# Performance work log

Measured on AMD Instinct MI355X. Metric: run time of the kernel, lower is better.

## Reference

```python
import jax, jax.numpy as jnp
import numpy as np

NT = 128          # num_timesteps (reference query points)
E = 128           # embed_time
H = 128           # nhidden
NH = 1            # num_heads
F = 32            # feature_size
NS = 2            # num_states
EPS = 1e-5


def layer_norm(x, g, b):
    m = jnp.mean(x, axis=-1, keepdims=True)
    v = jnp.mean((x - m) ** 2, axis=-1, keepdims=True)
    return (x - m) * jax.lax.rsqrt(v + EPS) * g + b


def setup_inputs() -> dict:
    key = jax.random.key(0)
    ks = jax.random.split(key, 24)
    nrm = lambda k, s: (jax.random.normal(k, s) * 0.05).astype(jnp.float32)
    inp = {
        "input": jax.random.normal(ks[0], (8, F, 512), dtype=jnp.float32),
        "mask": jax.random.randint(ks[1], (8, F, 512), 0, 2).astype(jnp.float32),
        "timesteps": jnp.sort(jax.random.uniform(ks[2], (8, 512), dtype=jnp.float32), axis=-1),
        # time embedding
        "periodic_w": nrm(ks[3], (E - 1, 1)), "periodic_b": nrm(ks[4], (E - 1,)),
        "lin_w": nrm(ks[5], (1, 1)), "lin_b": nrm(ks[6], (1,)),
        # query / key projections + layer norms
        "q_w": nrm(ks[7], (E, E)), "q_b": nrm(ks[8], (E,)),
        "q_g": jnp.ones((E,), jnp.float32), "q_be": jnp.zeros((E,), jnp.float32),
        "k_w": nrm(ks[9], (E, E)), "k_b": nrm(ks[10], (E,)),
        "k_g": jnp.ones((E,), jnp.float32), "k_be": jnp.zeros((E,), jnp.float32),
        # attention_norm over h*2F channels, then output linear + LN to nhidden
        "attn_g": jnp.ones((NH * 2 * F,), jnp.float32), "attn_b": jnp.zeros((NH * 2 * F,), jnp.float32),
        "out_w": nrm(ks[11], (H, NH * 2 * F)), "out_b": nrm(ks[12], (H,)),
        "out_g": jnp.ones((H,), jnp.float32), "out_be": jnp.zeros((H,), jnp.float32),
        # GRU (torch gate order r, z, n)
        "gru_wih": nrm(ks[13], (3 * H, H)), "gru_whh": nrm(ks[14], (3 * H, H)),
        "gru_bih": nrm(ks[15], (3 * H,)), "gru_bhh": nrm(ks[16], (3 * H,)),
        # classifier MLP
        "c1_w": nrm(ks[17], (H, H)), "c1_b": nrm(ks[18], (H,)),
        "c2_w": nrm(ks[19], (H, H)), "c2_b": nrm(ks[20], (H,)),
        "c3_w": nrm(ks[21], (NS, H)), "c3_b": nrm(ks[22], (NS,)),
    }
    return inp


def time_embedding(tt, lin_w, lin_b, periodic_w, periodic_b):
    t = tt[..., None]                                   # (..., 1)
    out1 = t @ lin_w.T + lin_b                          # (..., 1)
    out2 = jnp.sin(t @ periodic_w.T + periodic_b)       # (..., E-1)
    return jnp.concatenate([out1, out2], axis=-1)       # (..., E)


def reference(input, mask, timesteps, periodic_w, periodic_b, lin_w, lin_b,
              q_w, q_b, q_g, q_be, k_w, k_b, k_g, k_be,
              attn_g, attn_b, out_w, out_b, out_g, out_be,
              gru_wih, gru_whh, gru_bih, gru_bhh,
              c1_w, c1_b, c2_w, c2_b, c3_w, c3_b):
    B = input.shape[0]
    x_in = jnp.transpose(input, (0, 2, 1))              # (B, T, F)
    m = 1.0 - jnp.transpose(mask, (0, 2, 1))            # (B, T, F)
    x_in = x_in * (m > 0).astype(x_in.dtype)
    x = jnp.concatenate([x_in, m], axis=-1)             # (B, T, 2F)
    mk = jnp.concatenate([m, m], axis=-1)               # (B, T, 2F)

    key_e = time_embedding(timesteps, lin_w, lin_b, periodic_w, periodic_b)        # (B, T, E)
    qtimes = jnp.linspace(0.0, 1.0, NT)
    query_e = time_embedding(qtimes[None], lin_w, lin_b, periodic_w, periodic_b)   # (1, NT, E)

    q = layer_norm(query_e @ q_w.T + q_b, q_g, q_be)    # (1, NT, E)
    k = layer_norm(key_e @ k_w.T + k_b, k_g, k_be)      # (B, T, E)

    etk = E // NH
    q = q.reshape(1, NT, NH, etk).transpose(0, 2, 1, 3)         # (1, h, NT, etk)
    k = k.reshape(B, -1, NH, etk).transpose(0, 2, 1, 3)         # (B, h, T, etk)

    scores = jnp.einsum("ahqd,bhkd->bhqk", q, k) / np.sqrt(etk)  # (B, h, NT, T)
    # per-channel masked softmax over keys: (B, h, NT, T, 2F)
    logits = jnp.where(mk[:, None, None, :, :] == 0, -1e9, scores[..., None])
    p_attn = jax.nn.softmax(logits, axis=-2)
    att = jnp.sum(p_attn * x[:, None, None, :, :], axis=-2)     # (B, h, NT, 2F)

    x2 = att.transpose(0, 2, 1, 3).reshape(B, NT, NH * 2 * F)
    x2 = layer_norm(x2, attn_g, attn_b)
    out = layer_norm(x2 @ out_w.T + out_b, out_g, out_be)       # (B, NT, H)

    # GRU over the NT reference timesteps, last hidden state
    seq = out.transpose(1, 0, 2)                                # (NT, B, H)
    h0 = jnp.zeros((B, H), out.dtype)

    def gru_step(h, x_t):
        gi = x_t @ gru_wih.T + gru_bih
        gh = h @ gru_whh.T + gru_bhh
        ir, iz, inn = jnp.split(gi, 3, axis=-1)
        hr, hz, hn = jnp.split(gh, 3, axis=-1)
        r = jax.nn.sigmoid(ir + hr)
        z = jax.nn.sigmoid(iz + hz)
        n = jnp.tanh(inn + r * hn)
        h_new = (1.0 - z) * n + z * h
        return h_new, None

    h_last, _ = jax.lax.scan(gru_step, h0, seq)

    h1 = jax.nn.relu(h_last @ c1_w.T + c1_b)
    h2 = jax.nn.relu(h1 @ c2_w.T + c2_b)
    return h2 @ c3_w.T + c3_b                                   # (B, num_states) logits
```

## Files before the change

### kernel.cpp

```cpp
#include <hip/hip_runtime.h>
#include <math.h>

#define LN_EPS 1e-5f

typedef _Float16 h2v __attribute__((ext_vector_type(2)));

__device__ __forceinline__ float dot4(float4 a, float4 b) {
    return a.x*b.x + a.y*b.y + a.z*b.z + a.w*b.w;
}
__device__ __forceinline__ void fma4(float4& a, float s, float4 v) {
    a.x += s*v.x; a.y += s*v.y; a.z += s*v.z; a.w += s*v.w;
}
__device__ __forceinline__ float fast_rcp(float x) {
    return __builtin_amdgcn_rcpf(x);
}
__device__ __forceinline__ float fast_sigmoid(float x) {
    return fast_rcp(1.f + __expf(-x));
}
__device__ __forceinline__ float fast_tanh(float x) {
    return 1.f - 2.f*fast_rcp(__expf(2.f*x) + 1.f);
}
__device__ __forceinline__ float fdot2u(unsigned int a, unsigned int b, float c) {
#if __has_builtin(__builtin_amdgcn_fdot2)
    return __builtin_amdgcn_fdot2(__builtin_bit_cast(h2v, a),
                                  __builtin_bit_cast(h2v, b), c, false);
#else
    const h2v av = __builtin_bit_cast(h2v, a);
    const h2v bv = __builtin_bit_cast(h2v, b);
    return c + (float)av[0]*(float)bv[0] + (float)av[1]*(float)bv[1];
#endif
}
__device__ __forceinline__ float wsum64(float v) {
    #pragma unroll
    for (int off = 32; off > 0; off >>= 1) v += __shfl_xor(v, off);
    return v;
}
__device__ __forceinline__ float qadd_xor1(float v) {
    const int x = __builtin_amdgcn_mov_dpp(__builtin_bit_cast(int, v),
                                           0xB1 , 0xF, 0xF, true);
    return v + __builtin_bit_cast(float, x);
}

__global__ void k_embed_proj(
    const float* __restrict__ input, const float* __restrict__ mask,
    const float* __restrict__ timesteps,
    const float* __restrict__ pw, const float* __restrict__ pb,
    const float* __restrict__ lw, const float* __restrict__ lb,
    const float* __restrict__ q_w, const float* __restrict__ q_b,
    const float* __restrict__ q_g, const float* __restrict__ q_be,
    const float* __restrict__ k_w, const float* __restrict__ k_b,
    const float* __restrict__ k_g, const float* __restrict__ k_be,
    float* __restrict__ qs, float* __restrict__ kT, float2* __restrict__ xm)
{
    const int blk = blockIdx.x;
    const int tid = threadIdx.x;

    __shared__ __align__(16) float e[4][128];
    __shared__ __align__(16) float4 red[128];
    __shared__ __align__(16) float proj[4][128];
    __shared__ __align__(16) float2 tile[32][65];

    if (blk < 64) {
        const int b  = blk >> 3;
        const int t0 = (blk & 7) * 64;
        const int cg = tid >> 6;
        const int tt = tid & 63;
        #pragma unroll
        for (int c16 = 0; c16 < 16; ++c16) {
            const int c = c16*2 + cg;
            const float m = mask [(size_t)(b*32 + c)*512 + t0 + tt];
            const float x = input[(size_t)(b*32 + c)*512 + t0 + tt];
            const float mm = 1.0f - m;
            tile[c][tt] = make_float2(x*mm, mm);
        }
        __syncthreads();
        const int c2 = tid & 31;
        const int tg = tid >> 5;
        #pragma unroll
        for (int k = 0; k < 16; ++k) {
            const int t = tg*16 + k;
            xm[((size_t)b*512 + t0 + t)*32 + c2] = tile[c2][t];
        }
        return;
    }

    const bool isq = blk < 96;
    float tv[4];
    int kidx0 = 0;
    if (isq) {
        const int q0 = (blk - 64) * 4;
        #pragma unroll
        for (int r = 0; r < 4; ++r) tv[r] = (float)(q0 + r) * (1.0f/127.0f);
    } else {
        kidx0 = (blk - 96) * 4;
        #pragma unroll
        for (int r = 0; r < 4; ++r) tv[r] = timesteps[kidx0 + r];
    }

    float pwj = 0.f, pbj = 0.f;
    if (tid > 0) { pwj = pw[tid-1]; pbj = pb[tid-1]; }
    const float lw0 = lw[0], lb0 = lb[0];
    #pragma unroll
    for (int r = 0; r < 4; ++r)
        e[r][tid] = (tid == 0) ? (tv[r]*lw0 + lb0) : sinf(tv[r]*pwj + pbj);
    __syncthreads();

    const float* W  = isq ? q_w  : k_w;
    const float* Bv = isq ? q_b  : k_b;
    const float* G  = isq ? q_g  : k_g;
    const float* Be = isq ? q_be : k_be;

    {
        const int jj = tid >> 2, dc = tid & 3;
        const float4* e0 = (const float4*)(&e[0][0]);
        const float4* e1 = (const float4*)(&e[1][0]);
        const float4* e2 = (const float4*)(&e[2][0]);
        const float4* e3 = (const float4*)(&e[3][0]);
        #pragma unroll
        for (int jb = 0; jb < 4; ++jb) {
            const int j = jb*32 + jj;
            const float4* wrow = (const float4*)(W + (size_t)j*128);
            float a0=0.f, a1=0.f, a2=0.f, a3=0.f;
            #pragma unroll
            for (int k = 0; k < 8; ++k) {
                const int idx = dc + 4*k;
                const float4 w4 = wrow[idx];
                a0 += dot4(w4, e0[idx]);
                a1 += dot4(w4, e1[idx]);
                a2 += dot4(w4, e2[idx]);
                a3 += dot4(w4, e3[idx]);
            }
            a0 += __shfl_xor(a0, 1, 4); a0 += __shfl_xor(a0, 2, 4);
            a1 += __shfl_xor(a1, 1, 4); a1 += __shfl_xor(a1, 2, 4);
            a2 += __shfl_xor(a2, 1, 4); a2 += __shfl_xor(a2, 2, 4);
            a3 += __shfl_xor(a3, 1, 4); a3 += __shfl_xor(a3, 2, 4);
            if (dc == 0) {
                const float bj = Bv[j];
                proj[0][j] = a0 + bj; proj[1][j] = a1 + bj;
                proj[2][j] = a2 + bj; proj[3][j] = a3 + bj;
            }
        }
    }
    __syncthreads();

    float acc[4];
    #pragma unroll
    for (int r = 0; r < 4; ++r) acc[r] = proj[r][tid];

    red[tid] = make_float4(acc[0], acc[1], acc[2], acc[3]);
    __syncthreads();
    for (int s = 64; s > 0; s >>= 1) {
        if (tid < s) {
            float4 m = red[tid]; const float4 o = red[tid+s];
            m.x += o.x; m.y += o.y; m.z += o.z; m.w += o.w;
            red[tid] = m;
        }
        __syncthreads();
    }
    float4 mean = red[0];
    mean.x *= (1.0f/128.0f); mean.y *= (1.0f/128.0f);
    mean.z *= (1.0f/128.0f); mean.w *= (1.0f/128.0f);
    __syncthreads();
    const float d0 = acc[0]-mean.x, d1 = acc[1]-mean.y,
                d2 = acc[2]-mean.z, d3 = acc[3]-mean.w;
    red[tid] = make_float4(d0*d0, d1*d1, d2*d2, d3*d3);
    __syncthreads();
    for (int s = 64; s > 0; s >>= 1) {
        if (tid < s) {
            float4 m = red[tid]; const float4 o = red[tid+s];
            m.x += o.x; m.y += o.y; m.z += o.z; m.w += o.w;
            red[tid] = m;
        }
        __syncthreads();
    }
    float4 var = red[0];
    var.x *= (1.0f/128.0f); var.y *= (1.0f/128.0f);
    var.z *= (1.0f/128.0f); var.w *= (1.0f/128.0f);

    const float gg = G[tid], bb = Be[tid];
    const float o0 = d0*rsqrtf(var.x+LN_EPS)*gg + bb;
    const float o1 = d1*rsqrtf(var.y+LN_EPS)*gg + bb;
    const float o2 = d2*rsqrtf(var.z+LN_EPS)*gg + bb;
    const float o3 = d3*rsqrtf(var.w+LN_EPS)*gg + bb;

    if (isq) {
        const float sc = 0.08838834764831845f;
        const int q0 = (blk - 64)*4;
        qs[(size_t)(q0+0)*128 + tid] = o0*sc;
        qs[(size_t)(q0+1)*128 + tid] = o1*sc;
        qs[(size_t)(q0+2)*128 + tid] = o2*sc;
        qs[(size_t)(q0+3)*128 + tid] = o3*sc;
    } else {
        const int b = kidx0 >> 9;
        const int t = kidx0 & 511;
        *(float4*)(kT + ((size_t)(b*128 + tid))*512 + t) =
            make_float4(o0, o1, o2, o3);
    }
}

__global__ void __launch_bounds__(256) k_attn(
    const float2* __restrict__ xm,
    const float* __restrict__ qs, const float* __restrict__ kT,
    const float* __restrict__ attn_g, const float* __restrict__ attn_b,
    const float* __restrict__ out_w, const float* __restrict__ out_b,
    const float* __restrict__ out_g, const float* __restrict__ out_be,
    float* __restrict__ outm)
{
    const int b     = blockIdx.x >> 5;
    const int qbase = (blockIdx.x & 31) * 4;
    const int tid   = threadIdx.x;

    __shared__ __align__(16) float et[4][512];
    __shared__ __align__(16) float qsh[4][128];
    __shared__ __align__(16) float wsh[128*66];
    __shared__ __align__(16) float sA[4][8][32];
    __shared__ __align__(16) float aA[4][8][32];
    __shared__ __align__(16) float x2s[4][64];
    __shared__ float redC[4];

    for (int idx = tid; idx < 512; idx += 256)
        qsh[idx >> 7][idx & 127] = qs[(size_t)(qbase + (idx >> 7))*128 + (idx & 127)];
    for (int idx = tid; idx < 8192; idx += 256)
        wsh[(idx >> 6)*66 + (idx & 63)] = out_w[idx];
    __syncthreads();

    {
        const int grp = tid >> 7;
        const int tl  = tid & 127;
        const int q0  = grp*2;
        const float4* kp  = (const float4*)kT + (size_t)b*128*128 + tl;
        const float4* qa4 = (const float4*)qsh[q0];
        const float4* qb4 = (const float4*)qsh[q0+1];
        float4 a0 = make_float4(0,0,0,0), a1 = make_float4(0,0,0,0);
        float4 c0 = kp[0], c1 = kp[128], c2 = kp[256], c3 = kp[384];
        for (int c = 0; c < 32; ++c) {
            float4 n0, n1, n2, n3;
            if (c < 31) {
                const float4* kn = kp + (size_t)(4*c+4)*128;
                n0 = kn[0]; n1 = kn[128]; n2 = kn[256]; n3 = kn[384];
            }
            const float4 qa = qa4[c], qb = qb4[c];
            fma4(a0, qa.x, c0); fma4(a1, qb.x, c0);
            fma4(a0, qa.y, c1); fma4(a1, qb.y, c1);
            fma4(a0, qa.z, c2); fma4(a1, qb.z, c2);
            fma4(a0, qa.w, c3); fma4(a1, qb.w, c3);
            c0 = n0; c1 = n1; c2 = n2; c3 = n3;
        }
        a0.x = __expf(a0.x); a0.y = __expf(a0.y); a0.z = __expf(a0.z); a0.w = __expf(a0.w);
        a1.x = __expf(a1.x); a1.y = __expf(a1.y); a1.z = __expf(a1.z); a1.w = __expf(a1.w);
        ((float4*)et[q0])[tl]   = a0;
        ((float4*)et[q0+1])[tl] = a1;
    }
    __syncthreads();

    {
        const int c   = tid & 31;
        const int seg = tid >> 5;
        const float2* xp = xm + ((size_t)b*512 + seg*64)*32 + c;
        float s0=0,s1=0,s2=0,s3=0, a0=0,a1=0,a2=0,a3=0;
        #pragma unroll 4
        for (int i = 0; i < 64; ++i) {
            const float2 v = xp[(size_t)i*32];
            const int t = seg*64 + i;
            const float w0 = et[0][t]*v.y, w1 = et[1][t]*v.y;
            const float w2 = et[2][t]*v.y, w3 = et[3][t]*v.y;
            s0 += w0; s1 += w1; s2 += w2; s3 += w3;
            a0 += w0*v.x; a1 += w1*v.x; a2 += w2*v.x; a3 += w3*v.x;
        }
        sA[0][seg][c]=s0; sA[1][seg][c]=s1; sA[2][seg][c]=s2; sA[3][seg][c]=s3;
        aA[0][seg][c]=a0; aA[1][seg][c]=a1; aA[2][seg][c]=a2; aA[3][seg][c]=a3;
    }
    __syncthreads();

    {
        const int ql = tid >> 6;
        const int c2 = tid & 63;
        const int cc = c2 & 31;
        float ss = 0.f;
        #pragma unroll
        for (int g = 0; g < 8; ++g) ss += sA[ql][g][cc];
        float attv;
        if (c2 < 32) {
            float aa = 0.f;
            #pragma unroll
            for (int g = 0; g < 8; ++g) aa += aA[ql][g][cc];
            attv = (ss > 0.f) ? aa/ss : 0.f;
        } else {
            attv = (ss > 0.f) ? 1.0f : 0.0f;
        }
        const float mean = wsum64(attv) * (1.0f/64.0f);
        const float dv = attv - mean;
        const float var = wsum64(dv*dv) * (1.0f/64.0f);
        x2s[ql][c2] = dv*rsqrtf(var+LN_EPS)*attn_g[c2] + attn_b[c2];
    }
    __syncthreads();

    {
        const int jhalf = tid >> 7;
        const int j     = tid & 127;
        const int wave  = tid >> 6;
        for (int lq2 = 0; lq2 < 2; ++lq2) {
            const int ql = jhalf*2 + lq2;
            float acc = out_b[j];
            const float4* wrow = (const float4*)(wsh + j*66);
            const float4* xr   = (const float4*)x2s[ql];
            #pragma unroll
            for (int k = 0; k < 16; ++k) acc += dot4(wrow[k], xr[k]);

            float v = wsum64(acc);
            if ((tid & 63) == 0) redC[wave] = v;
            __syncthreads();
            const float mean = (redC[jhalf*2] + redC[jhalf*2+1]) * (1.0f/128.0f);
            __syncthreads();
            const float d = acc - mean;
            v = wsum64(d*d);
            if ((tid & 63) == 0) redC[wave] = v;
            __syncthreads();
            const float var = (redC[jhalf*2] + redC[jhalf*2+1]) * (1.0f/128.0f);
            outm[((size_t)b*128 + qbase + ql)*128 + j] =
                d*rsqrtf(var+LN_EPS)*out_g[j] + out_be[j];
            __syncthreads();
        }
    }
}

__global__ void k_gi(const float* __restrict__ outm,
                     const float* __restrict__ wih, const float* __restrict__ bih,
                     float* __restrict__ gi)
{
    const int qi  = blockIdx.x;
    const int tid = threadIdx.x;
    __shared__ __align__(16) float rows[8][128];
    for (int idx = tid; idx < 1024; idx += 384) {
        const int b = idx >> 7, d = idx & 127;
        rows[b][d] = outm[(size_t)(b*128+qi)*128 + d];
    }
    __syncthreads();

    const int g0 = tid >> 2, dc = tid & 3;
    #pragma unroll
    for (int gb = 0; gb < 4; ++gb) {
        const int g = gb*96 + g0;
        const float4* wrow = (const float4*)(wih + (size_t)g*128);
        float acc[8] = {0,0,0,0,0,0,0,0};
        #pragma unroll
        for (int k = 0; k < 8; ++k) {
            const int idx = dc + 4*k;
            const float4 w4 = wrow[idx];
            #pragma unroll
            for (int b = 0; b < 8; ++b)
                acc[b] += dot4(w4, ((const float4*)rows[b])[idx]);
        }
        #pragma unroll
        for (int b = 0; b < 8; ++b) {
            acc[b] += __shfl_xor(acc[b], 1, 4);
            acc[b] += __shfl_xor(acc[b], 2, 4);
        }
        if (dc == 0) {
            const float bi = bih[g];
            #pragma unroll
            for (int b = 0; b < 8; ++b)
                gi[((size_t)qi*8 + b)*384 + g] = acc[b] + bi;
        }
    }
}

__global__ void __launch_bounds__(256) k_gru_cls(
    const float* __restrict__ gi,
    const float* __restrict__ whh, const float* __restrict__ bhh,
    const float* __restrict__ c1w, const float* __restrict__ c1b,
    const float* __restrict__ c2w, const float* __restrict__ c2b,
    const float* __restrict__ c3w, const float* __restrict__ c3b,
    float* __restrict__ out)
{
    const int b   = blockIdx.x;
    const int tid = threadIdx.x;
    const int u   = tid >> 1;
    const int s   = tid & 1;

    __shared__ __align__(16) _Float16 hbuf[2][128];
    __shared__ __align__(16) float hcls[128];
    __shared__ __align__(16) float scr[256];

    unsigned int wreg[3][32];
    #pragma unroll
    for (int g = 0; g < 3; ++g) {
        const float4* wrow = (const float4*)(whh + (size_t)(g*128 + u)*128 + 64*s);
        #pragma unroll
        for (int i = 0; i < 16; ++i) {
            const float4 v = wrow[i];
            h2v p0; p0[0] = (_Float16)v.x; p0[1] = (_Float16)v.y;
            h2v p1; p1[0] = (_Float16)v.z; p1[1] = (_Float16)v.w;
            wreg[g][2*i]   = __builtin_bit_cast(unsigned int, p0);
            wreg[g][2*i+1] = __builtin_bit_cast(unsigned int, p1);
        }
    }
    const float bh_r = bhh[u], bh_z = bhh[u+128], bh_n = bhh[u+256];

    const float* gpR = gi + (size_t)b*384 + u;
    const float* gpZ = gpR + 128;
    const float* gpN = gpR + 256;

    float gR[4], gZ[4], gN[4];
    #pragma unroll
    for (int j = 0; j < 4; ++j) {
        gR[j] = gpR[(size_t)j*3072];
        gZ[j] = gpZ[(size_t)j*3072];
        gN[j] = gpN[(size_t)j*3072];
    }

    if (tid < 128) { hbuf[0][tid] = (_Float16)0.f; hbuf[1][tid] = (_Float16)0.f; }
    float hprev = 0.f;
    __syncthreads();

#define GRU_BODY(RB, WB, J, PF)                                                \
    {                                                                          \
        const float giR = gR[J], giZ = gZ[J], giN = gN[J];                     \
        gR[J] = gpR[(size_t)(PF)*3072];                                        \
        gZ[J] = gpZ[(size_t)(PF)*3072];                                        \
        gN[J] = gpN[(size_t)(PF)*3072];                                        \
        const uint4* hp4 = (const uint4*)&hbuf[RB][0] + s*8;                   \
        uint4 hv[8];                                                           \
        _Pragma("unroll")                                                      \
        for (int i = 0; i < 8; ++i) hv[i] = hp4[i];                            \
        float ar[2] = {0.f,0.f}, az[2] = {0.f,0.f}, an[2] = {0.f,0.f};         \
        _Pragma("unroll")                                                      \
        for (int i = 0; i < 8; ++i) {                                          \
            const int p = i >> 2;                                              \
            ar[p] = fdot2u(wreg[0][4*i+0], hv[i].x, ar[p]);                    \
            ar[p] = fdot2u(wreg[0][4*i+1], hv[i].y, ar[p]);                    \
            ar[p] = fdot2u(wreg[0][4*i+2], hv[i].z, ar[p]);                    \
            ar[p] = fdot2u(wreg[0][4*i+3], hv[i].w, ar[p]);                    \
            az[p] = fdot2u(wreg[1][4*i+0], hv[i].x, az[p]);                    \
            az[p] = fdot2u(wreg[1][4*i+1], hv[i].y, az[p]);                    \
            az[p] = fdot2u(wreg[1][4*i+2], hv[i].z, az[p]);                    \
            az[p] = fdot2u(wreg[1][4*i+3], hv[i].w, az[p]);                    \
            an[p] = fdot2u(wreg[2][4*i+0], hv[i].x, an[p]);                    \
            an[p] = fdot2u(wreg[2][4*i+1], hv[i].y, an[p]);                    \
            an[p] = fdot2u(wreg[2][4*i+2], hv[i].z, an[p]);                    \
            an[p] = fdot2u(wreg[2][4*i+3], hv[i].w, an[p]);                    \
        }                                                                      \
        float arr = qadd_xor1(ar[0] + ar[1]);                                  \
        float azz = qadd_xor1(az[0] + az[1]);                                  \
        float ann = qadd_xor1(an[0] + an[1]);                                  \
        const float r = fast_sigmoid(giR + arr + bh_r);                        \
        const float z = fast_sigmoid(giZ + azz + bh_z);                        \
        const float n = fast_tanh(giN + r*(ann + bh_n));                       \
        hprev = (1.f - z)*n + z*hprev;                                         \
        if (s == 0) hbuf[WB][u] = (_Float16)hprev;                             \
    }

    #pragma unroll 1
    for (int qi = 0; qi < 128; qi += 4) {
        GRU_BODY(0, 1, 0, (qi+4 < 128 ? qi+4 : 127));
        __syncthreads();
        GRU_BODY(1, 0, 1, (qi+5 < 128 ? qi+5 : 127));
        __syncthreads();
        GRU_BODY(0, 1, 2, (qi+6 < 128 ? qi+6 : 127));
        __syncthreads();
        GRU_BODY(1, 0, 3, (qi+7 < 128 ? qi+7 : 127));
        __syncthreads();
    }
#undef GRU_BODY

    if (s == 0) hcls[u] = hprev;
    __syncthreads();
    if (tid < 128) {
        float acc = c1b[tid];
        const float4* wc = (const float4*)(c1w + (size_t)tid*128);
        const float4* v  = (const float4*)hcls;
        #pragma unroll
        for (int d4 = 0; d4 < 32; ++d4) acc += dot4(wc[d4], v[d4]);
        scr[tid] = fmaxf(acc, 0.f);
    }
    __syncthreads();
    if (tid < 128) {
        float acc = c2b[tid];
        const float4* wc = (const float4*)(c2w + (size_t)tid*128);
        const float4* v  = (const float4*)scr;
        #pragma unroll
        for (int d4 = 0; d4 < 32; ++d4) acc += dot4(wc[d4], v[d4]);
        scr[128 + tid] = fmaxf(acc, 0.f);
    }
    __syncthreads();
    if (tid < 2) {
        float acc = c3b[tid];
        const float4* wc = (const float4*)(c3w + (size_t)tid*128);
        const float4* v  = (const float4*)(scr + 128);
        #pragma unroll
        for (int d4 = 0; d4 < 32; ++d4) acc += dot4(wc[d4], v[d4]);
        out[(size_t)b*2 + tid] = acc;
    }
}

extern "C" void kernel_launch(void* const* d_in, const int* in_sizes, int n_in,
                              void* d_out, int out_size, void* d_ws, size_t ws_size,
                              hipStream_t stream)
{
    const float* input     = (const float*)d_in[0];
    const float* mask      = (const float*)d_in[1];
    const float* timesteps = (const float*)d_in[2];
    const float* pw        = (const float*)d_in[3];
    const float* pb        = (const float*)d_in[4];
    const float* lw        = (const float*)d_in[5];
    const float* lb        = (const float*)d_in[6];
    const float* q_w       = (const float*)d_in[7];
    const float* q_b       = (const float*)d_in[8];
    const float* q_g       = (const float*)d_in[9];
    const float* q_be      = (const float*)d_in[10];
    const float* k_w       = (const float*)d_in[11];
    const float* k_b       = (const float*)d_in[12];
    const float* k_g       = (const float*)d_in[13];
    const float* k_be      = (const float*)d_in[14];
    const float* attn_g    = (const float*)d_in[15];
    const float* attn_b    = (const float*)d_in[16];
    const float* out_w     = (const float*)d_in[17];
    const float* out_b     = (const float*)d_in[18];
    const float* out_g     = (const float*)d_in[19];
    const float* out_be    = (const float*)d_in[20];
    const float* gru_wih   = (const float*)d_in[21];
    const float* gru_whh   = (const float*)d_in[22];
    const float* gru_bih   = (const float*)d_in[23];
    const float* gru_bhh   = (const float*)d_in[24];
    const float* c1_w      = (const float*)d_in[25];
    const float* c1_b      = (const float*)d_in[26];
    const float* c2_w      = (const float*)d_in[27];
    const float* c2_b      = (const float*)d_in[28];
    const float* c3_w      = (const float*)d_in[29];
    const float* c3_b      = (const float*)d_in[30];

    float* ws   = (float*)d_ws;
    float*  qs   = ws;
    float*  kT   = qs   + 16384;
    float*  outm = kT   + 524288;
    float*  gi   = outm + 131072;
    float2* xm   = (float2*)(gi + 393216);

    k_embed_proj<<<1120, 128, 0, stream>>>(input, mask, timesteps,
                                           pw, pb, lw, lb,
                                           q_w, q_b, q_g, q_be,
                                           k_w, k_b, k_g, k_be, qs, kT, xm);
    k_attn<<<256, 256, 0, stream>>>(xm, qs, kT,
                                    attn_g, attn_b, out_w, out_b,
                                    out_g, out_be, outm);
    k_gi<<<128, 384, 0, stream>>>(outm, gru_wih, gru_bih, gi);
    k_gru_cls<<<8, 256, 0, stream>>>(gi, gru_whh, gru_bhh,
                                     c1_w, c1_b, c2_w, c2_b, c3_w, c3_b,
                                     (float*)d_out);
}
```

Measured before the change: 220.3 us.

## Restructure GRU to one thread per unit and use wave-shuffle LayerNorm reductions

The GRU recurrence kernel now uses 128 threads, each holding a full row of fp16 recurrent weights in registers. This removes the DPP cross-lane add per step, and the recurrent bias is folded into the prefetched input gates. The step loop is unrolled by two instead of four. Separately, the embedding kernel's LayerNorm moves from a shared-memory tree reduction to wave shuffles, sin uses the fast intrinsic, and the out_w shared-memory load in the attention kernel is moved after the first compute phase. The risks are higher register pressure from 192 weight registers per thread and a longer serial dot product per step, plus lower accuracy from __sinf.

```diff
diff --git a/kernel.cpp b/kernel.cpp
--- a/kernel.cpp
+++ b/kernel.cpp
@@ -34,11 +34,6 @@
     #pragma unroll
     for (int off = 32; off > 0; off >>= 1) v += __shfl_xor(v, off);
     return v;
-}
-__device__ __forceinline__ float qadd_xor1(float v) {
-    const int x = __builtin_amdgcn_mov_dpp(__builtin_bit_cast(int, v),
-                                           0xB1 , 0xF, 0xF, true);
-    return v + __builtin_bit_cast(float, x);
 }
 
 __global__ void k_embed_proj(
@@ -56,9 +51,10 @@
     const int tid = threadIdx.x;
 
     __shared__ __align__(16) float e[4][128];
-    __shared__ __align__(16) float4 red[128];
     __shared__ __align__(16) float proj[4][128];
     __shared__ __align__(16) float2 tile[32][65];
+    __shared__ __align__(16) float4 red2[2];
+    __shared__ __align__(16) float4 red2b[2];
 
     if (blk < 64) {
         const int b  = blk >> 3;
@@ -102,7 +98,7 @@
     const float lw0 = lw[0], lb0 = lb[0];
     #pragma unroll
     for (int r = 0; r < 4; ++r)
-        e[r][tid] = (tid == 0) ? (tv[r]*lw0 + lb0) : sinf(tv[r]*pwj + pbj);
+        e[r][tid] = (tid == 0) ? (tv[r]*lw0 + lb0) : __sinf(tv[r]*pwj + pbj);
     __syncthreads();
 
     const float* W  = isq ? q_w  : k_w;
@@ -147,35 +143,33 @@
     #pragma unroll
     for (int r = 0; r < 4; ++r) acc[r] = proj[r][tid];
 
-    red[tid] = make_float4(acc[0], acc[1], acc[2], acc[3]);
-    __syncthreads();
-    for (int s = 64; s > 0; s >>= 1) {
-        if (tid < s) {
-            float4 m = red[tid]; const float4 o = red[tid+s];
-            m.x += o.x; m.y += o.y; m.z += o.z; m.w += o.w;
-            red[tid] = m;
-        }
-        __syncthreads();
-    }
-    float4 mean = red[0];
-    mean.x *= (1.0f/128.0f); mean.y *= (1.0f/128.0f);
-    mean.z *= (1.0f/128.0f); mean.w *= (1.0f/128.0f);
-    __syncthreads();
+    {
+        float4 m4;
+        m4.x = wsum64(acc[0]); m4.y = wsum64(acc[1]);
+        m4.z = wsum64(acc[2]); m4.w = wsum64(acc[3]);
+        if ((tid & 63) == 0) red2[tid >> 6] = m4;
+    }
+    __syncthreads();
+    float4 mean;
+    mean.x = (red2[0].x + red2[1].x) * (1.0f/128.0f);
+    mean.y = (red2[0].y + red2[1].y) * (1.0f/128.0f);
+    mean.z = (red2[0].z + red2[1].z) * (1.0f/128.0f);
+    mean.w = (red2[0].w + red2[1].w) * (1.0f/128.0f);
+
     const float d0 = acc[0]-mean.x, d1 = acc[1]-mean.y,
                 d2 = acc[2]-mean.z, d3 = acc[3]-mean.w;
-    red[tid] = make_float4(d0*d0, d1*d1, d2*d2, d3*d3);
-    __syncthreads();
-    for (int s = 64; s > 0; s >>= 1) {
-        if (tid < s) {
-            float4 m = red[tid]; const float4 o = red[tid+s];
-            m.x += o.x; m.y += o.y; m.z += o.z; m.w += o.w;
-            red[tid] = m;
-        }
-        __syncthreads();
-    }
-    float4 var = red[0];
-    var.x *= (1.0f/128.0f); var.y *= (1.0f/128.0f);
-    var.z *= (1.0f/128.0f); var.w *= (1.0f/128.0f);
+    {
+        float4 s4;
+        s4.x = wsum64(d0*d0); s4.y = wsum64(d1*d1);
+        s4.z = wsum64(d2*d2); s4.w = wsum64(d3*d3);
+        if ((tid & 63) == 0) red2b[tid >> 6] = s4;
+    }
+    __syncthreads();
+    float4 var;
+    var.x = (red2b[0].x + red2b[1].x) * (1.0f/128.0f);
+    var.y = (red2b[0].y + red2b[1].y) * (1.0f/128.0f);
+    var.z = (red2b[0].z + red2b[1].z) * (1.0f/128.0f);
+    var.w = (red2b[0].w + red2b[1].w) * (1.0f/128.0f);
 
     const float gg = G[tid], bb = Be[tid];
     const float o0 = d0*rsqrtf(var.x+LN_EPS)*gg + bb;
@@ -220,8 +214,6 @@
 
     for (int idx = tid; idx < 512; idx += 256)
         qsh[idx >> 7][idx & 127] = qs[(size_t)(qbase + (idx >> 7))*128 + (idx & 127)];
-    for (int idx = tid; idx < 8192; idx += 256)
-        wsh[(idx >> 6)*66 + (idx & 63)] = out_w[idx];
     __syncthreads();
 
     {
@@ -251,6 +243,8 @@
         ((float4*)et[q0])[tl]   = a0;
         ((float4*)et[q0+1])[tl] = a1;
     }
+    for (int idx = tid; idx < 8192; idx += 256)
+        wsh[(idx >> 6)*66 + (idx & 63)] = out_w[idx];
     __syncthreads();
 
     {
@@ -365,7 +359,7 @@
     }
 }
 
-__global__ void __launch_bounds__(256) k_gru_cls(
+__global__ void __launch_bounds__(128, 1) k_gru_cls(
     const float* __restrict__ gi,
     const float* __restrict__ whh, const float* __restrict__ bhh,
     const float* __restrict__ c1w, const float* __restrict__ c1b,
@@ -375,19 +369,17 @@
 {
     const int b   = blockIdx.x;
     const int tid = threadIdx.x;
-    const int u   = tid >> 1;
-    const int s   = tid & 1;
 
     __shared__ __align__(16) _Float16 hbuf[2][128];
     __shared__ __align__(16) float hcls[128];
     __shared__ __align__(16) float scr[256];
 
-    unsigned int wreg[3][32];
+    unsigned int wreg[3][64];
     #pragma unroll
     for (int g = 0; g < 3; ++g) {
-        const float4* wrow = (const float4*)(whh + (size_t)(g*128 + u)*128 + 64*s);
-        #pragma unroll
-        for (int i = 0; i < 16; ++i) {
+        const float4* wrow = (const float4*)(whh + (size_t)(g*128 + tid)*128);
+        #pragma unroll
+        for (int i = 0; i < 32; ++i) {
             const float4 v = wrow[i];
             h2v p0; p0[0] = (_Float16)v.x; p0[1] = (_Float16)v.y;
             h2v p1; p1[0] = (_Float16)v.z; p1[1] = (_Float16)v.w;
@@ -395,77 +387,101 @@
             wreg[g][2*i+1] = __builtin_bit_cast(unsigned int, p1);
         }
     }
-    const float bh_r = bhh[u], bh_z = bhh[u+128], bh_n = bhh[u+256];
-
-    const float* gpR = gi + (size_t)b*384 + u;
+    const float bh_r = bhh[tid], bh_z = bhh[tid+128], bh_n = bhh[tid+256];
+
+    const float* gpR = gi + (size_t)b*384 + tid;
     const float* gpZ = gpR + 128;
     const float* gpN = gpR + 256;
 
-    float gR[4], gZ[4], gN[4];
-    #pragma unroll
-    for (int j = 0; j < 4; ++j) {
-        gR[j] = gpR[(size_t)j*3072];
-        gZ[j] = gpZ[(size_t)j*3072];
-        gN[j] = gpN[(size_t)j*3072];
-    }
-
-    if (tid < 128) { hbuf[0][tid] = (_Float16)0.f; hbuf[1][tid] = (_Float16)0.f; }
+    float gR0 = gpR[0]      + bh_r, gZ0 = gpZ[0]      + bh_z, gN0 = gpN[0];
+    float gR1 = gpR[3072]   + bh_r, gZ1 = gpZ[3072]   + bh_z, gN1 = gpN[3072];
+
+    hbuf[0][tid] = (_Float16)0.f; hbuf[1][tid] = (_Float16)0.f;
     float hprev = 0.f;
     __syncthreads();
 
-#define GRU_BODY(RB, WB, J, PF)                                                \
+#define GRU_BODY(RB, WB, GR, GZ, GN, PF)                                       \
     {                                                                          \
-        const float giR = gR[J], giZ = gZ[J], giN = gN[J];                     \
-        gR[J] = gpR[(size_t)(PF)*3072];                                        \
-        gZ[J] = gpZ[(size_t)(PF)*3072];                                        \
-        gN[J] = gpN[(size_t)(PF)*3072];                                        \
-        const uint4* hp4 = (const uint4*)&hbuf[RB][0] + s*8;                   \
-        uint4 hv[8];                                                           \
-        _Pragma("unroll")                                                      \
-        for (int i = 0; i < 8; ++i) hv[i] = hp4[i];                            \
+        const float giR = GR, giZ = GZ, giN = GN;                              \
+        GR = gpR[(size_t)(PF)*3072] + bh_r;                                    \
+        GZ = gpZ[(size_t)(PF)*3072] + bh_z;                                    \
+        GN = gpN[(size_t)(PF)*3072];                                           \
+        const uint4* hp4 = (const uint4*)&hbuf[RB][0];                         \
         float ar[2] = {0.f,0.f}, az[2] = {0.f,0.f}, an[2] = {0.f,0.f};         \
         _Pragma("unroll")                                                      \
-        for (int i = 0; i < 8; ++i) {                                          \
-            const int p = i >> 2;                                              \
-            ar[p] = fdot2u(wreg[0][4*i+0], hv[i].x, ar[p]);                    \
-            ar[p] = fdot2u(wreg[0][4*i+1], hv[i].y, ar[p]);                    \
-            ar[p] = fdot2u(wreg[0][4*i+2], hv[i].z, ar[p]);                    \
-            ar[p] = fdot2u(wreg[0][4*i+3], hv[i].w, ar[p]);                    \
-            az[p] = fdot2u(wreg[1][4*i+0], hv[i].x, az[p]);                    \
-            az[p] = fdot2u(wreg[1][4*i+1], hv[i].y, az[p]);                    \
-            az[p] = fdot2u(wreg[1][4*i+2], hv[i].z, az[p]);                    \
-            az[p] = fdot2u(wreg[1][4*i+3], hv[i].w, az[p]);                    \
-            an[p] = fdot2u(wreg[2][4*i+0], hv[i].x, an[p]);                    \
-            an[p] = fdot2u(wreg[2][4*i+1], hv[i].y, an[p]);                    \
-            an[p] = fdot2u(wreg[2][4*i+2], hv[i].z, an[p]);                    \
-            an[p] = fdot2u(wreg[2][4*i+3], hv[i].w, an[p]);                    \
+        for (int c = 0; c < 4; ++c) {                                          \
+            const int p = c >> 1;                                              \
+            const uint4 h0 = hp4[4*c+0], h1 = hp4[4*c+1];                      \
+            const uint4 h2 = hp4[4*c+2], h3 = hp4[4*c+3];                      \
+            const int wb = 16*c;                                               \
+            ar[p] = fdot2u(wreg[0][wb+ 0], h0.x, ar[p]);                       \
+            ar[p] = fdot2u(wreg[0][wb+ 1], h0.y, ar[p]);                       \
+            ar[p] = fdot2u(wreg[0][wb+ 2], h0.z, ar[p]);                       \
+            ar[p] = fdot2u(wreg[0][wb+ 3], h0.w, ar[p]);                       \
+            ar[p] = fdot2u(wreg[0][wb+ 4], h1.x, ar[p]);                       \
+            ar[p] = fdot2u(wreg[0][wb+ 5], h1.y, ar[p]);                       \
+            ar[p] = fdot2u(wreg[0][wb+ 6], h1.z, ar[p]);                       \
+            ar[p] = fdot2u(wreg[0][wb+ 7], h1.w, ar[p]);                       \
+            ar[p] = fdot2u(wreg[0][wb+ 8], h2.x, ar[p]);                       \
+            ar[p] = fdot2u(wreg[0][wb+ 9], h2.y, ar[p]);                       \
+            ar[p] = fdot2u(wreg[0][wb+10], h2.z, ar[p]);                       \
+            ar[p] = fdot2u(wreg[0][wb+11], h2.w, ar[p]);                       \
+            ar[p] = fdot2u(wreg[0][wb+12], h3.x, ar[p]);                       \
+            ar[p] = fdot2u(wreg[0][wb+13], h3.y, ar[p]);                       \
+            ar[p] = fdot2u(wreg[0][wb+14], h3.z, ar[p]);                       \
+            ar[p] = fdot2u(wreg[0][wb+15], h3.w, ar[p]);                       \
+            az[p] = fdot2u(wreg[1][wb+ 0], h0.x, az[p]);                       \
+            az[p] = fdot2u(wreg[1][wb+ 1], h0.y, az[p]);                       \
+            az[p] = fdot2u(wreg[1][wb+ 2], h0.z, az[p]);                       \
+            az[p] = fdot2u(wreg[1][wb+ 3], h0.w, az[p]);                       \
+            az[p] = fdot2u(wreg[1][wb+ 4], h1.x, az[p]);                       \
+            az[p] = fdot2u(wreg[1][wb+ 5], h1.y, az[p]);                       \
+            az[p] = fdot2u(wreg[1][wb+ 6], h1.z, az[p]);                       \
+            az[p] = fdot2u(wreg[1][wb+ 7], h1.w, az[p]);                       \
+            az[p] = fdot2u(wreg[1][wb+ 8], h2.x, az[p]);                       \
+            az[p] = fdot2u(wreg[1][wb+ 9], h2.y, az[p]);                       \
+            az[p] = fdot2u(wreg[1][wb+10], h2.z, az[p]);                       \
+            az[p] = fdot2u(wreg[1][wb+11], h2.w, az[p]);                       \
+            az[p] = fdot2u(wreg[1][wb+12], h3.x, az[p]);                       \
+            az[p] = fdot2u(wreg[1][wb+13], h3.y, az[p]);                       \
+            az[p] = fdot2u(wreg[1][wb+14], h3.z, az[p]);                       \
+            az[p] = fdot2u(wreg[1][wb+15], h3.w, az[p]);                       \
+            an[p] = fdot2u(wreg[2][wb+ 0], h0.x, an[p]);                       \
+            an[p] = fdot2u(wreg[2][wb+ 1], h0.y, an[p]);                       \
+            an[p] = fdot2u(wreg[2][wb+ 2], h0.z, an[p]);                       \
+            an[p] = fdot2u(wreg[2][wb+ 3], h0.w, an[p]);                       \
+            an[p] = fdot2u(wreg[2][wb+ 4], h1.x, an[p]);                       \
+            an[p] = fdot2u(wreg[2][wb+ 5], h1.y, an[p]);                       \
+            an[p] = fdot2u(wreg[2][wb+ 6], h1.z, an[p]);                       \
+            an[p] = fdot2u(wreg[2][wb+ 7], h1.w, an[p]);                       \
+            an[p] = fdot2u(wreg[2][wb+ 8], h2.x, an[p]);                       \
+            an[p] = fdot2u(wreg[2][wb+ 9], h2.y, an[p]);                       \
+            an[p] = fdot2u(wreg[2][wb+10], h2.z, an[p]);                       \
+            an[p] = fdot2u(wreg[2][wb+11], h2.w, an[p]);                       \
+            an[p] = fdot2u(wreg[2][wb+12], h3.x, an[p]);                       \
+            an[p] = fdot2u(wreg[2][wb+13], h3.y, an[p]);                       \
+            an[p] = fdot2u(wreg[2][wb+14], h3.z, an[p]);                       \
+            an[p] = fdot2u(wreg[2][wb+15], h3.w, an[p]);                       \
         }                                                                      \
-        float arr = qadd_xor1(ar[0] + ar[1]);                                  \
-        float azz = qadd_xor1(az[0] + az[1]);                                  \
-        float ann = qadd_xor1(an[0] + an[1]);                                  \
-        const float r = fast_sigmoid(giR + arr + bh_r);                        \
-        const float z = fast_sigmoid(giZ + azz + bh_z);                        \
-        const float n = fast_tanh(giN + r*(ann + bh_n));                       \
+        const float r = fast_sigmoid(giR + ar[0] + ar[1]);                     \
+        const float z = fast_sigmoid(giZ + az[0] + az[1]);                     \
+        const float n = fast_tanh(giN + r*(an[0] + an[1] + bh_n));             \
         hprev = (1.f - z)*n + z*hprev;                                         \
-        if (s == 0) hbuf[WB][u] = (_Float16)hprev;                             \
+        hbuf[WB][tid] = (_Float16)hprev;                                       \
     }
 
     #pragma unroll 1
-    for (int qi = 0; qi < 128; qi += 4) {
-        GRU_BODY(0, 1, 0, (qi+4 < 128 ? qi+4 : 127));
+    for (int qi = 0; qi < 128; qi += 2) {
+        GRU_BODY(0, 1, gR0, gZ0, gN0, (qi+2 < 128 ? qi+2 : 127));
         __syncthreads();
-        GRU_BODY(1, 0, 1, (qi+5 < 128 ? qi+5 : 127));
+        GRU_BODY(1, 0, gR1, gZ1, gN1, (qi+3 < 128 ? qi+3 : 127));
         __syncthreads();
-        GRU_BODY(0, 1, 2, (qi+6 < 128 ? qi+6 : 127));
-        __syncthreads();
-        GRU_BODY(1, 0, 3, (qi+7 < 128 ? qi+7 : 127));
-        __syncthreads();
     }
 #undef GRU_BODY
 
-    if (s == 0) hcls[u] = hprev;
-    __syncthreads();
-    if (tid < 128) {
+    hcls[tid] = hprev;
+    __syncthreads();
+    {
         float acc = c1b[tid];
         const float4* wc = (const float4*)(c1w + (size_t)tid*128);
         const float4* v  = (const float4*)hcls;
@@ -474,7 +490,7 @@
         scr[tid] = fmaxf(acc, 0.f);
     }
     __syncthreads();
-    if (tid < 128) {
+    {
         float acc = c2b[tid];
         const float4* wc = (const float4*)(c2w + (size_t)tid*128);
         const float4* v  = (const float4*)scr;
@@ -544,7 +560,7 @@
                                     attn_g, attn_b, out_w, out_b,
                                     out_g, out_be, outm);
     k_gi<<<128, 384, 0, stream>>>(outm, gru_wih, gru_bih, gi);
-    k_gru_cls<<<8, 256, 0, stream>>>(gi, gru_whh, gru_bhh,
+    k_gru_cls<<<8, 128, 0, stream>>>(gi, gru_whh, gru_bhh,
                                      c1_w, c1_b, c2_w, c2_b, c3_w, c3_b,
                                      (float*)d_out);
 }
```

New measurement: 244.6 us. +11.0%, slower.

## Use lightweight LDS barriers in GRU loop and wave-shuffle LayerNorm reductions

Applied to the files above, without the earlier changes.

In the GRU recurrence, full __syncthreads are replaced by a barrier that waits only on LDS counters, so global prefetch loads of the input gates stay in flight across steps. An empty asm forces the h-vector LDS loads to be issued together before the dot products. The embed/projection LayerNorm swaps its shared-memory tree reduction for 64-lane shuffle sums, and sinf becomes __sinf. The out_w staging copy is moved after the score computation, and the GRU kernel gets a launch-bounds occupancy hint. Risks: __sinf loses accuracy for larger arguments, and the custom barrier relies on correct manual memory ordering.

```diff
diff --git a/kernel.cpp b/kernel.cpp
--- a/kernel.cpp
+++ b/kernel.cpp
@@ -4,6 +4,7 @@
 #define LN_EPS 1e-5f
 
 typedef _Float16 h2v __attribute__((ext_vector_type(2)));
+typedef unsigned int u32x4 __attribute__((ext_vector_type(4)));
 
 __device__ __forceinline__ float dot4(float4 a, float4 b) {
     return a.x*b.x + a.y*b.y + a.z*b.z + a.w*b.w;
@@ -39,6 +40,11 @@
     const int x = __builtin_amdgcn_mov_dpp(__builtin_bit_cast(int, v),
                                            0xB1 , 0xF, 0xF, true);
     return v + __builtin_bit_cast(float, x);
+}
+__device__ __forceinline__ void lds_barrier() {
+    asm volatile("s_waitcnt lgkmcnt(0)" ::: "memory");
+    __builtin_amdgcn_s_barrier();
+    asm volatile("" ::: "memory");
 }
 
 __global__ void k_embed_proj(
@@ -56,9 +62,10 @@
     const int tid = threadIdx.x;
 
     __shared__ __align__(16) float e[4][128];
-    __shared__ __align__(16) float4 red[128];
     __shared__ __align__(16) float proj[4][128];
     __shared__ __align__(16) float2 tile[32][65];
+    __shared__ __align__(16) float4 red2[2];
+    __shared__ __align__(16) float4 red2b[2];
 
     if (blk < 64) {
         const int b  = blk >> 3;
@@ -102,7 +109,7 @@
     const float lw0 = lw[0], lb0 = lb[0];
     #pragma unroll
     for (int r = 0; r < 4; ++r)
-        e[r][tid] = (tid == 0) ? (tv[r]*lw0 + lb0) : sinf(tv[r]*pwj + pbj);
+        e[r][tid] = (tid == 0) ? (tv[r]*lw0 + lb0) : __sinf(tv[r]*pwj + pbj);
     __syncthreads();
 
     const float* W  = isq ? q_w  : k_w;
@@ -147,35 +154,33 @@
     #pragma unroll
     for (int r = 0; r < 4; ++r) acc[r] = proj[r][tid];
 
-    red[tid] = make_float4(acc[0], acc[1], acc[2], acc[3]);
-    __syncthreads();
-    for (int s = 64; s > 0; s >>= 1) {
-        if (tid < s) {
-            float4 m = red[tid]; const float4 o = red[tid+s];
-            m.x += o.x; m.y += o.y; m.z += o.z; m.w += o.w;
-            red[tid] = m;
-        }
-        __syncthreads();
-    }
-    float4 mean = red[0];
-    mean.x *= (1.0f/128.0f); mean.y *= (1.0f/128.0f);
-    mean.z *= (1.0f/128.0f); mean.w *= (1.0f/128.0f);
-    __syncthreads();
+    {
+        float4 m4;
+        m4.x = wsum64(acc[0]); m4.y = wsum64(acc[1]);
+        m4.z = wsum64(acc[2]); m4.w = wsum64(acc[3]);
+        if ((tid & 63) == 0) red2[tid >> 6] = m4;
+    }
+    __syncthreads();
+    float4 mean;
+    mean.x = (red2[0].x + red2[1].x) * (1.0f/128.0f);
+    mean.y = (red2[0].y + red2[1].y) * (1.0f/128.0f);
+    mean.z = (red2[0].z + red2[1].z) * (1.0f/128.0f);
+    mean.w = (red2[0].w + red2[1].w) * (1.0f/128.0f);
+
     const float d0 = acc[0]-mean.x, d1 = acc[1]-mean.y,
                 d2 = acc[2]-mean.z, d3 = acc[3]-mean.w;
-    red[tid] = make_float4(d0*d0, d1*d1, d2*d2, d3*d3);
-    __syncthreads();
-    for (int s = 64; s > 0; s >>= 1) {
-        if (tid < s) {
-            float4 m = red[tid]; const float4 o = red[tid+s];
-            m.x += o.x; m.y += o.y; m.z += o.z; m.w += o.w;
-            red[tid] = m;
-        }
-        __syncthreads();
-    }
-    float4 var = red[0];
-    var.x *= (1.0f/128.0f); var.y *= (1.0f/128.0f);
-    var.z *= (1.0f/128.0f); var.w *= (1.0f/128.0f);
+    {
+        float4 s4;
+        s4.x = wsum64(d0*d0); s4.y = wsum64(d1*d1);
+        s4.z = wsum64(d2*d2); s4.w = wsum64(d3*d3);
+        if ((tid & 63) == 0) red2b[tid >> 6] = s4;
+    }
+    __syncthreads();
+    float4 var;
+    var.x = (red2b[0].x + red2b[1].x) * (1.0f/128.0f);
+    var.y = (red2b[0].y + red2b[1].y) * (1.0f/128.0f);
+    var.z = (red2b[0].z + red2b[1].z) * (1.0f/128.0f);
+    var.w = (red2b[0].w + red2b[1].w) * (1.0f/128.0f);
 
     const float gg = G[tid], bb = Be[tid];
     const float o0 = d0*rsqrtf(var.x+LN_EPS)*gg + bb;
@@ -220,8 +225,6 @@
 
     for (int idx = tid; idx < 512; idx += 256)
         qsh[idx >> 7][idx & 127] = qs[(size_t)(qbase + (idx >> 7))*128 + (idx & 127)];
-    for (int idx = tid; idx < 8192; idx += 256)
-        wsh[(idx >> 6)*66 + (idx & 63)] = out_w[idx];
     __syncthreads();
 
     {
@@ -251,6 +254,8 @@
         ((float4*)et[q0])[tl]   = a0;
         ((float4*)et[q0+1])[tl] = a1;
     }
+    for (int idx = tid; idx < 8192; idx += 256)
+        wsh[(idx >> 6)*66 + (idx & 63)] = out_w[idx];
     __syncthreads();
 
     {
@@ -365,7 +370,7 @@
     }
 }
 
-__global__ void __launch_bounds__(256) k_gru_cls(
+__global__ void __launch_bounds__(256, 1) k_gru_cls(
     const float* __restrict__ gi,
     const float* __restrict__ whh, const float* __restrict__ bhh,
     const float* __restrict__ c1w, const float* __restrict__ c1b,
@@ -419,10 +424,18 @@
         gR[J] = gpR[(size_t)(PF)*3072];                                        \
         gZ[J] = gpZ[(size_t)(PF)*3072];                                        \
         gN[J] = gpN[(size_t)(PF)*3072];                                        \
-        const uint4* hp4 = (const uint4*)&hbuf[RB][0] + s*8;                   \
-        uint4 hv[8];                                                           \
+        const u32x4* hp4 = (const u32x4*)&hbuf[RB][0] + s*8;                   \
+        u32x4 hv[8];                                                           \
         _Pragma("unroll")                                                      \
         for (int i = 0; i < 8; ++i) hv[i] = hp4[i];                            \
+        asm volatile("" :: "v"(hv[0].x), "v"(hv[0].y), "v"(hv[0].z), "v"(hv[0].w), \
+                           "v"(hv[1].x), "v"(hv[1].y), "v"(hv[1].z), "v"(hv[1].w), \
+                           "v"(hv[2].x), "v"(hv[2].y), "v"(hv[2].z), "v"(hv[2].w), \
+                           "v"(hv[3].x), "v"(hv[3].y), "v"(hv[3].z), "v"(hv[3].w)); \
+        asm volatile("" :: "v"(hv[4].x), "v"(hv[4].y), "v"(hv[4].z), "v"(hv[4].w), \
+                           "v"(hv[5].x), "v"(hv[5].y), "v"(hv[5].z), "v"(hv[5].w), \
+                           "v"(hv[6].x), "v"(hv[6].y), "v"(hv[6].z), "v"(hv[6].w), \
+                           "v"(hv[7].x), "v"(hv[7].y), "v"(hv[7].z), "v"(hv[7].w)); \
         float ar[2] = {0.f,0.f}, az[2] = {0.f,0.f}, an[2] = {0.f,0.f};         \
         _Pragma("unroll")                                                      \
         for (int i = 0; i < 8; ++i) {                                          \
@@ -440,9 +453,9 @@
             an[p] = fdot2u(wreg[2][4*i+2], hv[i].z, an[p]);                    \
             an[p] = fdot2u(wreg[2][4*i+3], hv[i].w, an[p]);                    \
         }                                                                      \
-        float arr = qadd_xor1(ar[0] + ar[1]);                                  \
-        float azz = qadd_xor1(az[0] + az[1]);                                  \
-        float ann = qadd_xor1(an[0] + an[1]);                                  \
+        const float arr = qadd_xor1(ar[0] + ar[1]);                            \
+        const float azz = qadd_xor1(az[0] + az[1]);                            \
+        const float ann = qadd_xor1(an[0] + an[1]);                            \
         const float r = fast_sigmoid(giR + arr + bh_r);                        \
         const float z = fast_sigmoid(giZ + azz + bh_z);                        \
         const float n = fast_tanh(giN + r*(ann + bh_n));                       \
@@ -453,13 +466,13 @@
     #pragma unroll 1
     for (int qi = 0; qi < 128; qi += 4) {
         GRU_BODY(0, 1, 0, (qi+4 < 128 ? qi+4 : 127));
-        __syncthreads();
+        lds_barrier();
         GRU_BODY(1, 0, 1, (qi+5 < 128 ? qi+5 : 127));
-        __syncthreads();
+        lds_barrier();
         GRU_BODY(0, 1, 2, (qi+6 < 128 ? qi+6 : 127));
-        __syncthreads();
+        lds_barrier();
         GRU_BODY(1, 0, 3, (qi+7 < 128 ? qi+7 : 127));
-        __syncthreads();
+        lds_barrier();
     }
 #undef GRU_BODY
 
```

New measurement: 225.8 us. +2.5%, slower.
